# Optimization experiments

Hardware: AMD Instinct MI355X
Metric: run time of the kernel (lower is better)

The kernel has to match this reference:

```python
import jax, jax.numpy as jnp
import numpy as np

B, L, P, D, C, S = 32768, 256, 1024, 50, 3, 10  # batch, latent, n_protos, proto_size, classes, slots/class
EPS = 1e-5
IN_EPS = 1e-5  # torch InstanceNorm1d default eps


def _instance_norm(h):
    # torch InstanceNorm1d on (N, 50): unbatched (C, L) semantics -> normalize each row
    # over the feature axis with biased variance, no affine.
    m = jnp.mean(h, axis=-1, keepdims=True)
    v = jnp.mean((h - m) ** 2, axis=-1, keepdims=True)
    return (h - m) * jax.lax.rsqrt(v + IN_EPS)


def _project(z, W1, b1, W2, b2):
    # Linear(256->50) -> InstanceNorm1d -> ReLU -> Linear(50->50)
    h = z @ W1.T + b1
    h = jax.nn.relu(_instance_norm(h))
    return h @ W2.T + b2


def setup_inputs() -> dict:
    key = jax.random.key(0)
    ks = jax.random.split(key, 6)
    x = jax.random.normal(ks[0], (B, L), dtype=jnp.float32)
    prototypes = jax.random.normal(ks[1], (P, L), dtype=jnp.float32)
    # xavier_normal_(gain=1) on (C, P, S): std = sqrt(2 / (fan_in + fan_out)) = sqrt(2/(P+S))
    proto_presence = jax.random.normal(ks[2], (C, P, S), dtype=jnp.float32) * np.sqrt(2.0 / (P + S)).astype(np.float32)
    W1 = jax.random.normal(ks[3], (D, L), dtype=jnp.float32) * np.sqrt(1.0 / L).astype(np.float32)
    b1 = jnp.zeros((D,), jnp.float32)
    W2 = jax.random.normal(ks[4], (D, D), dtype=jnp.float32) * np.sqrt(1.0 / D).astype(np.float32)
    b2 = jnp.zeros((D,), jnp.float32)
    # class_identity_layer weight: Wc[c, i] = 1 if i // S == c else 0  -> (C, C*S)
    Wc = jnp.asarray((np.arange(C * S) // S == np.arange(C)[:, None]).astype(np.float32))
    return {"x": x, "gumbel_scalar": 0, "prototypes": prototypes,
            "proto_presence": proto_presence, "W1": W1, "b1": b1,
            "W2": W2, "b2": b2, "Wc": Wc}


def reference(x, gumbel_scalar, prototypes, proto_presence, W1, b1, W2, b2, Wc):
    # routing weights over prototypes (dim=1)
    if gumbel_scalar == 0:
        pp = jax.nn.softmax(proto_presence, axis=1)
    else:
        u = jax.random.uniform(jax.random.key(1), proto_presence.shape,
                               minval=1e-20, maxval=1.0, dtype=proto_presence.dtype)
        g = -jnp.log(-jnp.log(u))
        pp = jax.nn.softmax((proto_presence * gumbel_scalar + g) / 0.5, axis=1)

    xp = _project(x, W1, b1, W2, b2)            # [B, 50]
    lp = _project(prototypes, W1, b1, W2, b2)   # [P, 50] (batched per-prototype loop; row-wise InstanceNorm is identical)

    # L2 distance via ||a-b||^2 = ||a||^2 + ||b||^2 - 2 a.b (single GEMM instead of [B,50,P] broadcast)
    l2 = (jnp.sum(xp * xp, axis=-1)[:, None]
          + jnp.sum(lp * lp, axis=-1)[None, :]
          - 2.0 * (xp @ lp.T))                  # [B, P]
    l2 = jnp.maximum(l2, 0.0)  # clamp tiny negative fp residue; exact math is >= 0

    similarity = jnp.log((l2 + 1.0) / (l2 + EPS))          # [B, P]
    mixed = jnp.einsum('bp,cpn->bcn', similarity, pp)      # [B, C, S]
    out1 = mixed.reshape(x.shape[0], -1) @ Wc.T            # [B, C]
    out2 = jnp.concatenate([jnp.tanh(out1[:, :1]), jax.nn.relu(out1[:, 1:])], axis=1)
    return (out2, xp, similarity, pp)
```

## Files before the change

### kernel.cpp

```cpp
#include <hip/hip_runtime.h>
#include <cmath>

#define Bn 32768
#define Ln 256
#define Pn 1024
#define Dn 50
#define Cn 3
#define Sn 10

typedef short bf16x8 __attribute__((ext_vector_type(8)));
typedef float f32x4 __attribute__((ext_vector_type(4)));

__device__ inline unsigned short f2bf(float f) {
    unsigned int u = __float_as_uint(f);
    unsigned int r = (u + 0x7FFFu + ((u >> 16) & 1u)) >> 16;
    return (unsigned short)r;
}

__global__ void pp_softmax_kernel(const float* __restrict__ pres, float* __restrict__ pp) {
    int c = blockIdx.x / Sn;
    int n = blockIdx.x % Sn;
    int lane = threadIdx.x;
    const float* src = pres + (size_t)c * Pn * Sn + n;
    float* dst = pp + (size_t)c * Pn * Sn + n;
    float v[16];
    float mx = -1e30f;
#pragma unroll
    for (int i = 0; i < 16; ++i) { v[i] = src[(size_t)(lane + i * 64) * Sn]; mx = fmaxf(mx, v[i]); }
#pragma unroll
    for (int m = 1; m < 64; m <<= 1) mx = fmaxf(mx, __shfl_xor(mx, m, 64));
    float sum = 0.f;
#pragma unroll
    for (int i = 0; i < 16; ++i) { v[i] = __expf(v[i] - mx); sum += v[i]; }
#pragma unroll
    for (int m = 1; m < 64; m <<= 1) sum += __shfl_xor(sum, m, 64);
    float inv = 1.0f / sum;
#pragma unroll
    for (int i = 0; i < 16; ++i) dst[(size_t)(lane + i * 64) * Sn] = v[i] * inv;
}

__global__ void pp_rowsum_kernel(const float* __restrict__ pp, float* __restrict__ pps) {
    int idx = blockIdx.x * blockDim.x + threadIdx.x;
    if (idx < Cn * Pn) {
        float s = 0.f;
#pragma unroll
        for (int n = 0; n < Sn; ++n) s += pp[(size_t)idx * Sn + n];
        pps[idx] = s;
    }
}

__global__ __launch_bounds__(256) void project_kernel(
    const float* __restrict__ zin,
    const float* __restrict__ W1, const float* __restrict__ b1,
    const float* __restrict__ W2, const float* __restrict__ b2,
    float* __restrict__ outp, float* __restrict__ outn,
    unsigned short* __restrict__ outb)
{
    __shared__ float xs[64][68];
    __shared__ float w1t[64][68];
    __shared__ float w2t[52][68];

    int t = threadIdx.x;
    int tx = t & 15, ty = t >> 4;
    int row0 = blockIdx.x * 64;

    for (int idx = t; idx < 52 * 64; idx += 256) {
        int j = idx & 63, k = idx >> 6;
        w2t[k][j] = (j < Dn && k < Dn) ? W2[j * Dn + k] : 0.f;
    }

    float acc[4][4] = {};
    for (int kc = 0; kc < Ln; kc += 64) {
        __syncthreads();
        for (int idx = t; idx < 64 * 64; idx += 256) {
            int kk = idx & 63, r = idx >> 6;
            xs[r][kk] = zin[(size_t)(row0 + r) * Ln + kc + kk];
        }
        for (int idx = t; idx < 64 * 64; idx += 256) {
            int j = idx & 63, kk = idx >> 6;
            w1t[kk][j] = (j < Dn) ? W1[j * Ln + kc + kk] : 0.f;
        }
        __syncthreads();
#pragma unroll 4
        for (int k4 = 0; k4 < 16; ++k4) {
            float4 xv[4], wv[4];
#pragma unroll
            for (int i = 0; i < 4; ++i) xv[i] = *(const float4*)&xs[ty * 4 + i][k4 * 4];
#pragma unroll
            for (int kk = 0; kk < 4; ++kk) wv[kk] = *(const float4*)&w1t[k4 * 4 + kk][tx * 4];
#pragma unroll
            for (int i = 0; i < 4; ++i)
#pragma unroll
                for (int kk = 0; kk < 4; ++kk)
#pragma unroll
                    for (int j = 0; j < 4; ++j)
                        acc[i][j] += (&xv[i].x)[kk] * (&wv[kk].x)[j];
        }
    }

    float rb1[4], rb2[4];
    bool valid[4];
#pragma unroll
    for (int j = 0; j < 4; ++j) {
        int c = tx * 4 + j;
        valid[j] = c < Dn;
        rb1[j] = valid[j] ? b1[c] : 0.f;
        rb2[j] = valid[j] ? b2[c] : 0.f;
    }

    __syncthreads();

#pragma unroll
    for (int i = 0; i < 4; ++i) {
        float h[4];
        float s = 0.f;
#pragma unroll
        for (int j = 0; j < 4; ++j) { h[j] = acc[i][j] + rb1[j]; s += h[j]; }
#pragma unroll
        for (int m = 1; m < 16; m <<= 1) s += __shfl_xor(s, m, 64);
        float mean = s * (1.0f / Dn);
        float s2 = 0.f;
#pragma unroll
        for (int j = 0; j < 4; ++j) { float dv = valid[j] ? (h[j] - mean) : 0.f; s2 += dv * dv; }
#pragma unroll
        for (int m = 1; m < 16; m <<= 1) s2 += __shfl_xor(s2, m, 64);
        float rstd = rsqrtf(s2 * (1.0f / Dn) + 1e-5f);
        float4 rv;
#pragma unroll
        for (int j = 0; j < 4; ++j)
            (&rv.x)[j] = valid[j] ? fmaxf((h[j] - mean) * rstd, 0.f) : 0.f;
        *(float4*)&xs[ty * 4 + i][tx * 4] = rv;
    }
    __syncthreads();

    float acc2[4][4] = {};
#pragma unroll 4
    for (int k4 = 0; k4 < 13; ++k4) {
        float4 xv[4], wv[4];
#pragma unroll
        for (int i = 0; i < 4; ++i) xv[i] = *(const float4*)&xs[ty * 4 + i][k4 * 4];
#pragma unroll
        for (int kk = 0; kk < 4; ++kk) wv[kk] = *(const float4*)&w2t[k4 * 4 + kk][tx * 4];
#pragma unroll
        for (int i = 0; i < 4; ++i)
#pragma unroll
            for (int kk = 0; kk < 4; ++kk)
#pragma unroll
                for (int j = 0; j < 4; ++j)
                    acc2[i][j] += (&xv[i].x)[kk] * (&wv[kk].x)[j];
    }

#pragma unroll
    for (int i = 0; i < 4; ++i) {
        int row = row0 + ty * 4 + i;
        float o[4];
        float q = 0.f;
#pragma unroll
        for (int j = 0; j < 4; ++j) {
            o[j] = acc2[i][j] + rb2[j];
            if (valid[j]) q += o[j] * o[j];
            if (valid[j]) outp[(size_t)row * Dn + tx * 4 + j] = o[j];
        }
        ushort4 ob;
        ob.x = valid[0] ? f2bf(o[0]) : 0;
        ob.y = valid[1] ? f2bf(o[1]) : 0;
        ob.z = valid[2] ? f2bf(o[2]) : 0;
        ob.w = valid[3] ? f2bf(o[3]) : 0;
        *(ushort4*)&outb[(size_t)row * 64 + tx * 4] = ob;
#pragma unroll
        for (int m = 1; m < 16; m <<= 1) q += __shfl_xor(q, m, 64);
        if (tx == 0) outn[row] = q;
    }
}

__global__ __launch_bounds__(256) void sim_mfma_kernel(
    const unsigned short* __restrict__ xpb, const unsigned short* __restrict__ lpb,
    const float* __restrict__ xpn, const float* __restrict__ lpn,
    const float* __restrict__ pps,
    float* __restrict__ sim, float* __restrict__ out1)
{
    int t = threadIdx.x;
    int w = t >> 6, l = t & 63;
    int lr = l & 15, lg = l >> 4;
    int row0 = blockIdx.x * 64;

    bf16x8 af[4][2];
#pragma unroll
    for (int m = 0; m < 4; ++m)
#pragma unroll
        for (int ks = 0; ks < 2; ++ks)
            af[m][ks] = *(const bf16x8*)&xpb[(size_t)(row0 + m * 16 + lr) * 64 + ks * 32 + lg * 8];

    float xnr[4][4];
#pragma unroll
    for (int m = 0; m < 4; ++m)
#pragma unroll
        for (int i = 0; i < 4; ++i)
            xnr[m][i] = xpn[row0 + m * 16 + lg * 4 + i];

    float oacc[4][4][3] = {};

    for (int pt = 0; pt < 4; ++pt) {
#pragma unroll
        for (int n = 0; n < 4; ++n) {
            int pc = w * 256 + pt * 64 + n * 16;
            bf16x8 bfr[2];
#pragma unroll
            for (int ks = 0; ks < 2; ++ks)
                bfr[ks] = *(const bf16x8*)&lpb[(size_t)(pc + lr) * 64 + ks * 32 + lg * 8];
            f32x4 acc[4];
#pragma unroll
            for (int m = 0; m < 4; ++m) { f32x4 z = {0.f, 0.f, 0.f, 0.f}; acc[m] = z; }
#pragma unroll
            for (int ks = 0; ks < 2; ++ks)
#pragma unroll
                for (int m = 0; m < 4; ++m)
                    acc[m] = __builtin_amdgcn_mfma_f32_16x16x32_bf16(af[m][ks], bfr[ks], acc[m], 0, 0, 0);

            float ln = lpn[pc + lr];
            float pr0 = pps[pc + lr];
            float pr1 = pps[Pn + pc + lr];
            float pr2 = pps[2 * Pn + pc + lr];
#pragma unroll
            for (int m = 0; m < 4; ++m)
#pragma unroll
                for (int i = 0; i < 4; ++i) {
                    float l2 = xnr[m][i] + ln - 2.f * acc[m][i];
                    l2 = fmaxf(l2, 0.f);
                    float s = __logf(__fdividef(l2 + 1.f, l2 + 1e-5f));
                    sim[(size_t)(row0 + m * 16 + lg * 4 + i) * Pn + pc + lr] = s;
                    oacc[m][i][0] += s * pr0;
                    oacc[m][i][1] += s * pr1;
                    oacc[m][i][2] += s * pr2;
                }
        }
    }

#pragma unroll
    for (int m = 0; m < 4; ++m)
#pragma unroll
        for (int i = 0; i < 4; ++i)
#pragma unroll
            for (int c = 0; c < 3; ++c) {
                float v = oacc[m][i][c];
                v += __shfl_xor(v, 1, 64);
                v += __shfl_xor(v, 2, 64);
                v += __shfl_xor(v, 4, 64);
                v += __shfl_xor(v, 8, 64);
                if (lr == 0)
                    atomicAdd(&out1[(size_t)(row0 + m * 16 + lg * 4 + i) * Cn + c], v);
            }
}

__global__ void finalize_kernel(const float* __restrict__ o1, float* __restrict__ out2) {
    int i = blockIdx.x * 256 + threadIdx.x;
    if (i < Bn * Cn) {
        float v = o1[i];
        int c = i - (i / Cn) * Cn;
        out2[i] = (c == 0) ? tanhf(v) : fmaxf(v, 0.f);
    }
}

extern "C" void kernel_launch(void* const* d_in, const int* in_sizes, int n_in,
                              void* d_out, int out_size, void* d_ws, size_t ws_size,
                              hipStream_t stream) {
    const float* x    = (const float*)d_in[0];
    const float* prot = (const float*)d_in[2];
    const float* pres = (const float*)d_in[3];
    const float* W1   = (const float*)d_in[4];
    const float* b1   = (const float*)d_in[5];
    const float* W2   = (const float*)d_in[6];
    const float* b2   = (const float*)d_in[7];

    float* out  = (float*)d_out;
    float* out2 = out;
    float* xp   = out + (size_t)Bn * Cn;
    float* sim  = xp + (size_t)Bn * Dn;
    float* pp   = sim + (size_t)Bn * Pn;

    float* ws     = (float*)d_ws;
    float* out1ws = ws;
    float* xpn    = out1ws + (size_t)Bn * Cn;
    float* lpn    = xpn + Bn;
    float* pps    = lpn + Pn;
    float* lpf    = pps + Cn * Pn;
    unsigned short* xpb = (unsigned short*)(lpf + Pn * Dn);
    unsigned short* lpb = xpb + (size_t)Bn * 64;

    hipMemsetAsync(out1ws, 0, (size_t)Bn * Cn * sizeof(float), stream);
    hipLaunchKernelGGL(pp_softmax_kernel, dim3(Cn * Sn), dim3(64), 0, stream, pres, pp);
    hipLaunchKernelGGL(pp_rowsum_kernel, dim3((Cn * Pn + 255) / 256), dim3(256), 0, stream, pp, pps);
    hipLaunchKernelGGL(project_kernel, dim3(Bn / 64), dim3(256), 0, stream,
                       x, W1, b1, W2, b2, xp, xpn, xpb);
    hipLaunchKernelGGL(project_kernel, dim3(Pn / 64), dim3(256), 0, stream,
                       prot, W1, b1, W2, b2, lpf, lpn, lpb);
    hipLaunchKernelGGL(sim_mfma_kernel, dim3(Bn / 64), dim3(256), 0, stream,
                       xpb, lpb, xpn, lpn, pps, sim, out1ws);
    hipLaunchKernelGGL(finalize_kernel, dim3((Bn * Cn + 255) / 256), dim3(256), 0, stream,
                       out1ws, out2);
}
```

Before: 325.2 us.

## Fuse softmax row-sum via atomics, halve sim tile rows, prefetch prototype fragments

The separate pp row-sum kernel is removed. The softmax kernel now accumulates per-prototype sums into a zeroed workspace with atomics, and a single widened memset clears that workspace together with out1. The similarity kernel now processes 32 rows per block instead of 64, doubling the grid and declaring a min-blocks-per-CU launch bound for more occupancy. It also double-buffers the prototype bf16 fragments and norms/weights across 16-wide steps to hide load latency. The costs are float atomics, which make the row sums order-nondeterministic, and less reuse of each prototype fragment loaded per block.

```diff
diff --git a/kernel.cpp b/kernel.cpp
--- a/kernel.cpp
+++ b/kernel.cpp
@@ -17,7 +17,8 @@
     return (unsigned short)r;
 }
 
-__global__ void pp_softmax_kernel(const float* __restrict__ pres, float* __restrict__ pp) {
+__global__ void pp_softmax_kernel(const float* __restrict__ pres, float* __restrict__ pp,
+                                  float* __restrict__ pps) {
     int c = blockIdx.x / Sn;
     int n = blockIdx.x % Sn;
     int lane = threadIdx.x;
@@ -36,16 +37,10 @@
     for (int m = 1; m < 64; m <<= 1) sum += __shfl_xor(sum, m, 64);
     float inv = 1.0f / sum;
 #pragma unroll
-    for (int i = 0; i < 16; ++i) dst[(size_t)(lane + i * 64) * Sn] = v[i] * inv;
-}
-
-__global__ void pp_rowsum_kernel(const float* __restrict__ pp, float* __restrict__ pps) {
-    int idx = blockIdx.x * blockDim.x + threadIdx.x;
-    if (idx < Cn * Pn) {
-        float s = 0.f;
-#pragma unroll
-        for (int n = 0; n < Sn; ++n) s += pp[(size_t)idx * Sn + n];
-        pps[idx] = s;
+    for (int i = 0; i < 16; ++i) {
+        float r = v[i] * inv;
+        dst[(size_t)(lane + i * 64) * Sn] = r;
+        atomicAdd(&pps[c * Pn + lane + i * 64], r);
     }
 }
 
@@ -173,7 +168,7 @@
     }
 }
 
-__global__ __launch_bounds__(256) void sim_mfma_kernel(
+__global__ __launch_bounds__(256, 4) void sim_mfma_kernel(
     const unsigned short* __restrict__ xpb, const unsigned short* __restrict__ lpb,
     const float* __restrict__ xpn, const float* __restrict__ lpn,
     const float* __restrict__ pps,
@@ -182,62 +177,77 @@
     int t = threadIdx.x;
     int w = t >> 6, l = t & 63;
     int lr = l & 15, lg = l >> 4;
-    int row0 = blockIdx.x * 64;
-
-    bf16x8 af[4][2];
-#pragma unroll
-    for (int m = 0; m < 4; ++m)
+    int row0 = blockIdx.x * 32;
+
+    bf16x8 af[2][2];
+#pragma unroll
+    for (int m = 0; m < 2; ++m)
 #pragma unroll
         for (int ks = 0; ks < 2; ++ks)
             af[m][ks] = *(const bf16x8*)&xpb[(size_t)(row0 + m * 16 + lr) * 64 + ks * 32 + lg * 8];
 
-    float xnr[4][4];
-#pragma unroll
-    for (int m = 0; m < 4; ++m)
+    float xnr[2][4];
+#pragma unroll
+    for (int m = 0; m < 2; ++m)
 #pragma unroll
         for (int i = 0; i < 4; ++i)
             xnr[m][i] = xpn[row0 + m * 16 + lg * 4 + i];
 
-    float oacc[4][4][3] = {};
-
-    for (int pt = 0; pt < 4; ++pt) {
-#pragma unroll
-        for (int n = 0; n < 4; ++n) {
-            int pc = w * 256 + pt * 64 + n * 16;
-            bf16x8 bfr[2];
+    float oacc[2][4][3] = {};
+
+    bf16x8 bfr[2][2];
+    float lnv[2], p0v[2], p1v[2], p2v[2];
+    {
+        int pc = w * 256;
+#pragma unroll
+        for (int ks = 0; ks < 2; ++ks)
+            bfr[0][ks] = *(const bf16x8*)&lpb[(size_t)(pc + lr) * 64 + ks * 32 + lg * 8];
+        lnv[0] = lpn[pc + lr];
+        p0v[0] = pps[pc + lr];
+        p1v[0] = pps[Pn + pc + lr];
+        p2v[0] = pps[2 * Pn + pc + lr];
+    }
+
+    for (int tt = 0; tt < 16; ++tt) {
+        int cur = tt & 1, nxt = cur ^ 1;
+        if (tt < 15) {
+            int pc = w * 256 + (tt + 1) * 16;
 #pragma unroll
             for (int ks = 0; ks < 2; ++ks)
-                bfr[ks] = *(const bf16x8*)&lpb[(size_t)(pc + lr) * 64 + ks * 32 + lg * 8];
-            f32x4 acc[4];
-#pragma unroll
-            for (int m = 0; m < 4; ++m) { f32x4 z = {0.f, 0.f, 0.f, 0.f}; acc[m] = z; }
-#pragma unroll
-            for (int ks = 0; ks < 2; ++ks)
-#pragma unroll
-                for (int m = 0; m < 4; ++m)
-                    acc[m] = __builtin_amdgcn_mfma_f32_16x16x32_bf16(af[m][ks], bfr[ks], acc[m], 0, 0, 0);
-
-            float ln = lpn[pc + lr];
-            float pr0 = pps[pc + lr];
-            float pr1 = pps[Pn + pc + lr];
-            float pr2 = pps[2 * Pn + pc + lr];
-#pragma unroll
-            for (int m = 0; m < 4; ++m)
-#pragma unroll
-                for (int i = 0; i < 4; ++i) {
-                    float l2 = xnr[m][i] + ln - 2.f * acc[m][i];
-                    l2 = fmaxf(l2, 0.f);
-                    float s = __logf(__fdividef(l2 + 1.f, l2 + 1e-5f));
-                    sim[(size_t)(row0 + m * 16 + lg * 4 + i) * Pn + pc + lr] = s;
-                    oacc[m][i][0] += s * pr0;
-                    oacc[m][i][1] += s * pr1;
-                    oacc[m][i][2] += s * pr2;
-                }
-        }
-    }
-
-#pragma unroll
-    for (int m = 0; m < 4; ++m)
+                bfr[nxt][ks] = *(const bf16x8*)&lpb[(size_t)(pc + lr) * 64 + ks * 32 + lg * 8];
+            lnv[nxt] = lpn[pc + lr];
+            p0v[nxt] = pps[pc + lr];
+            p1v[nxt] = pps[Pn + pc + lr];
+            p2v[nxt] = pps[2 * Pn + pc + lr];
+        }
+        int pc = w * 256 + tt * 16;
+
+        f32x4 acc[2];
+#pragma unroll
+        for (int m = 0; m < 2; ++m) { f32x4 z = {0.f, 0.f, 0.f, 0.f}; acc[m] = z; }
+#pragma unroll
+        for (int ks = 0; ks < 2; ++ks)
+#pragma unroll
+            for (int m = 0; m < 2; ++m)
+                acc[m] = __builtin_amdgcn_mfma_f32_16x16x32_bf16(af[m][ks], bfr[cur][ks], acc[m], 0, 0, 0);
+
+        float ln = lnv[cur], pr0 = p0v[cur], pr1 = p1v[cur], pr2 = p2v[cur];
+#pragma unroll
+        for (int m = 0; m < 2; ++m)
+#pragma unroll
+            for (int i = 0; i < 4; ++i) {
+                float l2 = xnr[m][i] + ln - 2.f * acc[m][i];
+                l2 = fmaxf(l2, 0.f);
+                float s = __logf(__fdividef(l2 + 1.f, l2 + 1e-5f));
+                sim[(size_t)(row0 + m * 16 + lg * 4 + i) * Pn + pc + lr] = s;
+                oacc[m][i][0] += s * pr0;
+                oacc[m][i][1] += s * pr1;
+                oacc[m][i][2] += s * pr2;
+            }
+    }
+
+#pragma unroll
+    for (int m = 0; m < 2; ++m)
 #pragma unroll
         for (int i = 0; i < 4; ++i)
 #pragma unroll
@@ -280,21 +290,20 @@
 
     float* ws     = (float*)d_ws;
     float* out1ws = ws;
-    float* xpn    = out1ws + (size_t)Bn * Cn;
+    float* pps    = out1ws + (size_t)Bn * Cn;
+    float* xpn    = pps + Cn * Pn;
     float* lpn    = xpn + Bn;
-    float* pps    = lpn + Pn;
-    float* lpf    = pps + Cn * Pn;
+    float* lpf    = lpn + Pn;
     unsigned short* xpb = (unsigned short*)(lpf + Pn * Dn);
     unsigned short* lpb = xpb + (size_t)Bn * 64;
 
-    hipMemsetAsync(out1ws, 0, (size_t)Bn * Cn * sizeof(float), stream);
-    hipLaunchKernelGGL(pp_softmax_kernel, dim3(Cn * Sn), dim3(64), 0, stream, pres, pp);
-    hipLaunchKernelGGL(pp_rowsum_kernel, dim3((Cn * Pn + 255) / 256), dim3(256), 0, stream, pp, pps);
+    hipMemsetAsync(out1ws, 0, ((size_t)Bn * Cn + Cn * Pn) * sizeof(float), stream);
+    hipLaunchKernelGGL(pp_softmax_kernel, dim3(Cn * Sn), dim3(64), 0, stream, pres, pp, pps);
     hipLaunchKernelGGL(project_kernel, dim3(Bn / 64), dim3(256), 0, stream,
                        x, W1, b1, W2, b2, xp, xpn, xpb);
     hipLaunchKernelGGL(project_kernel, dim3(Pn / 64), dim3(256), 0, stream,
                        prot, W1, b1, W2, b2, lpf, lpn, lpb);
-    hipLaunchKernelGGL(sim_mfma_kernel, dim3(Bn / 64), dim3(256), 0, stream,
+    hipLaunchKernelGGL(sim_mfma_kernel, dim3(Bn / 32), dim3(256), 0, stream,
                        xpb, lpb, xpn, lpn, pps, sim, out1ws);
     hipLaunchKernelGGL(finalize_kernel, dim3((Bn * Cn + 255) / 256), dim3(256), 0, stream,
                        out1ws, out2);
```

New measurement: 683.5 us. +110.2%, slower.
